# Kernel optimization log

Hardware: AMD Instinct MI355X
Metric: run time of the kernel (lower is better)

## Reference

```python
import jax, jax.numpy as jnp
import numpy as np

B, M, D = 2048, 40, 64          # batch, num fields, embedding dim
HIDDEN = [128, 128, 128]        # CIN layer sizes


def setup_inputs() -> dict:
    key = jax.random.key(0)
    kx, k0, k1, k2 = jax.random.split(key, 4)
    x = jax.random.normal(kx, (B, M, D), dtype=jnp.float32)
    # torch.rand -> uniform [0, 1)
    W0 = jax.random.uniform(k0, (M, M, HIDDEN[0]), dtype=jnp.float32)
    W1 = jax.random.uniform(k1, (M, HIDDEN[0], HIDDEN[1]), dtype=jnp.float32)
    W2 = jax.random.uniform(k2, (M, HIDDEN[1], HIDDEN[2]), dtype=jnp.float32)
    return {"x": x, "W0": W0, "W1": W1, "W2": W2}


def _cin_forward(x, Ws):
    # x: [b, m, d]. Each layer k:
    #   x_next[b, l, d] = sum_{m, h} x0[b, m, d] * x_k[b, h, d] * W_k[m, h, l]
    # which equals the torch 'bil,bjl->bjil' outer product followed by
    # 'bijk,ijl->bkl' + transpose, but expressed as one fused contraction
    # (opt_einsum picks a path avoiding the worst intermediate).
    ps = []
    xk = x  # [b, H_k, d], H_0 = m
    for W in Ws:
        x_next = jnp.einsum('bmd,bhd,mhl->bld', x, xk, W)  # [b, L_k, d]
        ps.append(jnp.sum(x_next, axis=2))                  # [b, L_k]
        xk = x_next
    return jnp.concatenate(ps, axis=1)                      # [b, sum(L_k)]


def reference(x, W0, W1, W2):
    return _cin_forward(x, (W0, W1, W2))
```

## Files before the change

kernel.cpp:

```cpp
#include <hip/hip_runtime.h>
#include <hip/hip_bf16.h>
#include <cstdint>

#define BATCH 2048
#define MF    40
#define DDIM  64
#define LDIM  128
#define ROWS  (BATCH * DDIM)

typedef __attribute__((ext_vector_type(4)))  short    short4_t;
typedef __attribute__((ext_vector_type(8)))  short    short8;
typedef __attribute__((ext_vector_type(8)))  __bf16   bf16x8;
typedef __attribute__((ext_vector_type(2)))  float    floatx2;
typedef __attribute__((ext_vector_type(16))) float    floatx16;

__device__ __forceinline__ unsigned short f32_to_bf16(float f) {
    union { float f; uint32_t u; } v; v.f = f;
    uint32_t u = v.u;
    uint32_t r = (u + 0x7fffu + ((u >> 16) & 1u)) >> 16;
    return (unsigned short)r;
}

__device__ __forceinline__ void barrier_raw() {
    asm volatile("s_barrier" ::: "memory");
}
template <int N> __device__ __forceinline__ void vmwait() {
    if constexpr (N == 0)  asm volatile("s_waitcnt vmcnt(0)"  ::: "memory");
    if constexpr (N == 3)  asm volatile("s_waitcnt vmcnt(3)"  ::: "memory");
    if constexpr (N == 4)  asm volatile("s_waitcnt vmcnt(4)"  ::: "memory");
    if constexpr (N == 10) asm volatile("s_waitcnt vmcnt(10)" ::: "memory");
}

__global__ void k_wprep(const float* __restrict__ W, unsigned short* __restrict__ Wt,
                        int KK, int H) {
    int bi = blockIdx.x;
    int lane = threadIdx.x;
    int cb = bi & 3;
    int mkk = bi >> 2;
    int kk = mkk % KK, m = mkk / KK;
    int l = cb * 32 + (lane & 31);
    int hbase = kk * 16 + (lane >> 5) * 8;
    unsigned short o[8];
#pragma unroll
    for (int j = 0; j < 8; ++j) {
        int h = hbase + j;
        float v = (h < H) ? W[((size_t)m * H + h) * LDIM + l] : 0.f;
        o[j] = f32_to_bf16(v);
    }
    *(short8*)(Wt + ((size_t)bi * 64 + lane) * 8) = *(const short8*)o;
}

template <int KK, int KU, bool FIRST, int OFF, bool WRITEX>
__global__ __launch_bounds__(256, 2) void k_gemm(
    const float* __restrict__ x,
    const unsigned short* __restrict__ Xprev,
    const unsigned short* __restrict__ Wt,
    unsigned short* __restrict__ Xout,
    float* __restrict__ out)
{
    constexpr int UPM   = KK / KU;
    constexpr int NU    = MF * UPM;
    constexpr int SLOTS = (KU == 4) ? 2 : 3;
    constexpr int DIST  = SLOTS;

    __shared__ unsigned short slab[4][KU * 2048];

    const int tid  = threadIdx.x;
    const int lane = tid & 63, wave = tid >> 6;
    const int hf   = lane >> 5, r31 = lane & 31;
    const int rowhalf = wave >> 1, colhalf = wave & 1;
    const int b = blockIdx.x * 2 + rowhalf;

    bf16x8 xk[2][KK];
    if constexpr (FIRST) {
#pragma unroll
        for (int t = 0; t < 2; ++t)
#pragma unroll
            for (int kk = 0; kk < KK; ++kk) {
                unsigned short tmp[8];
#pragma unroll
                for (int j = 0; j < 8; ++j) {
                    int h = kk * 16 + hf * 8 + j;
                    float v = (h < MF) ? x[((size_t)b * MF + h) * DDIM + t * 32 + r31] : 0.f;
                    tmp[j] = f32_to_bf16(v);
                }
                xk[t][kk] = __builtin_bit_cast(bf16x8, *(const short8*)tmp);
            }
    } else {
#pragma unroll
        for (int t = 0; t < 2; ++t)
#pragma unroll
            for (int kk = 0; kk < KK; ++kk)
                xk[t][kk] = __builtin_bit_cast(bf16x8, *(const short8*)(
                    Xprev + (size_t)(b * 64 + t * 32 + r31) * LDIM + kk * 16 + hf * 8));
    }

    floatx16 acc[2][2] = {};

    auto stage = [&](int uu) {
        int u = uu < NU ? uu : NU - 1;
        const unsigned short* src = Wt + (size_t)u * (KU * 2048);
#pragma unroll
        for (int it = 0; it < KU; ++it) {
            int c = it * 256 + tid;
            __builtin_amdgcn_global_load_lds(
                (const __attribute__((address_space(1))) uint32_t*)(src + (size_t)c * 8),
                (__attribute__((address_space(3))) uint32_t*)(&slab[u & 3][(size_t)c * 8]),
                16, 0, 0);
        }
    };

    const int cbg0 = colhalf * 2, cbg1 = colhalf * 2 + 1;
    auto ldfrag = [&](int u, int frag, int cb) {
        return __builtin_bit_cast(bf16x8,
            *(const short8*)(&slab[u & 3][((size_t)(frag * 4 + cb) * 64 + lane) * 8]));
    };

    vmwait<0>();
    stage(0); stage(1); stage(2);
    vmwait<(KU == 4) ? 4 : 3>();
    barrier_raw();

    bf16x8 bbuf[SLOTS][2];
#pragma unroll
    for (int p = 0; p < SLOTS; ++p) {
        bbuf[p][0] = ldfrag(0, p, cbg0);
        bbuf[p][1] = ldfrag(0, p, cbg1);
    }

    float s0v = 0.f, s1v = 0.f;

#pragma unroll 1
    for (int m = 0; m < MF; ++m) {
        floatx16 P[2][2] = {};
#pragma unroll
        for (int kk = 0; kk < KK; ++kk) {
            if (kk % KU == 0) {
                barrier_raw();
                asm volatile("s_setprio 1");
                if (kk == 0) {
                    const float* sp = x + ((size_t)b * MF + m) * DDIM + r31;
                    s0v = sp[0];
                    s1v = sp[32];
                }
                stage(m * UPM + kk / KU + 3);
            }
            const int slot = (KU == 4) ? (kk & 1) : kk;
            P[0][0] = __builtin_amdgcn_mfma_f32_32x32x16_bf16(bbuf[slot][0], xk[0][kk], P[0][0], 0, 0, 0);
            P[1][0] = __builtin_amdgcn_mfma_f32_32x32x16_bf16(bbuf[slot][0], xk[1][kk], P[1][0], 0, 0, 0);
            P[0][1] = __builtin_amdgcn_mfma_f32_32x32x16_bf16(bbuf[slot][1], xk[0][kk], P[0][1], 0, 0, 0);
            P[1][1] = __builtin_amdgcn_mfma_f32_32x32x16_bf16(bbuf[slot][1], xk[1][kk], P[1][1], 0, 0, 0);
            {
                const int j  = kk + DIST;
                int mm = m + ((j >= KK) ? 1 : 0);
                if (mm > MF - 1) mm = MF - 1;
                const int jj = (j >= KK) ? (j - KK) : j;
                const int u  = mm * UPM + jj / KU;
                bbuf[slot][0] = ldfrag(u, jj % KU, cbg0);
                bbuf[slot][1] = ldfrag(u, jj % KU, cbg1);
            }
            if (kk % KU == KU - 1) vmwait<10>();
        }
        asm volatile("s_setprio 0");
#pragma unroll
        for (int t = 0; t < 2; ++t) {
            const float sv = (t == 0) ? s0v : s1v;
            floatx2 s2 = {sv, sv};
#pragma unroll
            for (int cbp = 0; cbp < 2; ++cbp) {
                floatx2*       A = (floatx2*)&acc[t][cbp];
                const floatx2* Q = (const floatx2*)&P[t][cbp];
#pragma unroll
                for (int i = 0; i < 8; ++i) A[i] += s2 * Q[i];
            }
        }
    }

    if constexpr (WRITEX) {
#pragma unroll
        for (int t = 0; t < 2; ++t) {
            const size_t rowbase = (size_t)(b * 64 + t * 32 + r31) * LDIM;
#pragma unroll
            for (int cbp = 0; cbp < 2; ++cbp) {
#pragma unroll
                for (int g = 0; g < 4; ++g) {
                    unsigned short o[4];
#pragma unroll
                    for (int i = 0; i < 4; ++i) o[i] = f32_to_bf16(acc[t][cbp][g * 4 + i]);
                    *(short4_t*)(Xout + rowbase + (colhalf * 2 + cbp) * 32 + 8 * g + 4 * hf) =
                        *(const short4_t*)o;
                }
            }
        }
    }

#pragma unroll
    for (int cbp = 0; cbp < 2; ++cbp) {
#pragma unroll
        for (int j = 0; j < 16; ++j) {
            float v = acc[0][cbp][j] + acc[1][cbp][j];
            v += __shfl_xor(v, 16);
            v += __shfl_xor(v, 8);
            v += __shfl_xor(v, 4);
            v += __shfl_xor(v, 2);
            v += __shfl_xor(v, 1);
            if (r31 == 0)
                out[(size_t)b * 384 + OFF + (colhalf * 2 + cbp) * 32 +
                    (j & 3) + 8 * (j >> 2) + 4 * hf] = v;
        }
    }
}

extern "C" void kernel_launch(void* const* d_in, const int* in_sizes, int n_in,
                              void* d_out, int out_size, void* d_ws, size_t ws_size,
                              hipStream_t stream) {
    const float* x  = (const float*)d_in[0];
    const float* W0 = (const float*)d_in[1];
    const float* W1 = (const float*)d_in[2];
    const float* W2 = (const float*)d_in[3];
    float* out = (float*)d_out;

    char* ws = (char*)d_ws;
    size_t off = 0;
    auto alloc = [&](size_t bytes) -> void* {
        void* p = ws + off;
        off += (bytes + 255) & ~(size_t)255;
        return p;
    };
    unsigned short* W0t = (unsigned short*)alloc((size_t)MF * 3 * 2048 * 2);
    unsigned short* W1t = (unsigned short*)alloc((size_t)MF * 8 * 2048 * 2);
    unsigned short* W2t = (unsigned short*)alloc((size_t)MF * 8 * 2048 * 2);
    unsigned short* X1p = (unsigned short*)alloc((size_t)ROWS * LDIM * 2);
    unsigned short* X2p = (unsigned short*)alloc((size_t)ROWS * LDIM * 2);

    k_wprep<<<MF * 3 * 4, 64, 0, stream>>>(W0, W0t, 3, 40);
    k_wprep<<<MF * 8 * 4, 64, 0, stream>>>(W1, W1t, 8, 128);
    k_wprep<<<MF * 8 * 4, 64, 0, stream>>>(W2, W2t, 8, 128);

    k_gemm<3, 3, true,  0,   true ><<<ROWS / 128, 256, 0, stream>>>(x, nullptr, W0t, X1p, out);
    k_gemm<8, 4, false, 128, true ><<<ROWS / 128, 256, 0, stream>>>(x, X1p,     W1t, X2p, out);
    k_gemm<8, 4, false, 256, false><<<ROWS / 128, 256, 0, stream>>>(x, X2p,     W2t, X2p, out);
}
```

Baseline: 463.2 us.

## Fuse three CIN layers into one kernel with LDS exchange of intermediates

```diff
diff --git a/kernel.cpp b/kernel.cpp
--- a/kernel.cpp
+++ b/kernel.cpp
@@ -24,16 +24,26 @@
 __device__ __forceinline__ void barrier_raw() {
     asm volatile("s_barrier" ::: "memory");
 }
+__device__ __forceinline__ void lgkmwait0() {
+    asm volatile("s_waitcnt lgkmcnt(0)" ::: "memory");
+}
 template <int N> __device__ __forceinline__ void vmwait() {
     if constexpr (N == 0)  asm volatile("s_waitcnt vmcnt(0)"  ::: "memory");
-    if constexpr (N == 3)  asm volatile("s_waitcnt vmcnt(3)"  ::: "memory");
     if constexpr (N == 4)  asm volatile("s_waitcnt vmcnt(4)"  ::: "memory");
+    if constexpr (N == 6)  asm volatile("s_waitcnt vmcnt(6)"  ::: "memory");
     if constexpr (N == 10) asm volatile("s_waitcnt vmcnt(10)" ::: "memory");
 }
 
-__global__ void k_wprep(const float* __restrict__ W, unsigned short* __restrict__ Wt,
-                        int KK, int H) {
+__global__ void k_wprep_all(const float* __restrict__ W0, const float* __restrict__ W1,
+                            const float* __restrict__ W2,
+                            unsigned short* __restrict__ W0t,
+                            unsigned short* __restrict__ W1t,
+                            unsigned short* __restrict__ W2t) {
     int bi = blockIdx.x;
+    const float* W; unsigned short* Wt; int KK, H;
+    if (bi < 640)       { W = W0; Wt = W0t; KK = 4; H = 40; }
+    else if (bi < 1920) { bi -= 640;  W = W1; Wt = W1t; KK = 8; H = 128; }
+    else                { bi -= 1920; W = W2; Wt = W2t; KK = 8; H = 128; }
     int lane = threadIdx.x;
     int cb = bi & 3;
     int mkk = bi >> 2;
@@ -47,83 +57,50 @@
         float v = (h < H) ? W[((size_t)m * H + h) * LDIM + l] : 0.f;
         o[j] = f32_to_bf16(v);
     }
-    *(short8*)(Wt + ((size_t)bi * 64 + lane) * 8) = *(const short8*)o;
-}
-
-template <int KK, int KU, bool FIRST, int OFF, bool WRITEX>
-__global__ __launch_bounds__(256, 2) void k_gemm(
-    const float* __restrict__ x,
-    const unsigned short* __restrict__ Xprev,
+    *(short8*)(Wt + (((size_t)(m * KK + kk) * 4 + cb) * 64 + lane) * 8) = *(const short8*)o;
+}
+
+template <int KK>
+__device__ __forceinline__ void layer_loop(
     const unsigned short* __restrict__ Wt,
-    unsigned short* __restrict__ Xout,
-    float* __restrict__ out)
+    const float* __restrict__ x, int b,
+    int lane, int hf, int r31, int cbg0, int cbg1,
+    unsigned short* slabf,
+    bf16x8 (&xk)[2][8], floatx16 (&acc)[2][2])
 {
-    constexpr int UPM   = KK / KU;
-    constexpr int NU    = MF * UPM;
-    constexpr int SLOTS = (KU == 4) ? 2 : 3;
-    constexpr int DIST  = SLOTS;
-
-    __shared__ unsigned short slab[4][KU * 2048];
-
-    const int tid  = threadIdx.x;
-    const int lane = tid & 63, wave = tid >> 6;
-    const int hf   = lane >> 5, r31 = lane & 31;
-    const int rowhalf = wave >> 1, colhalf = wave & 1;
-    const int b = blockIdx.x * 2 + rowhalf;
-
-    bf16x8 xk[2][KK];
-    if constexpr (FIRST) {
-#pragma unroll
-        for (int t = 0; t < 2; ++t)
-#pragma unroll
-            for (int kk = 0; kk < KK; ++kk) {
-                unsigned short tmp[8];
-#pragma unroll
-                for (int j = 0; j < 8; ++j) {
-                    int h = kk * 16 + hf * 8 + j;
-                    float v = (h < MF) ? x[((size_t)b * MF + h) * DDIM + t * 32 + r31] : 0.f;
-                    tmp[j] = f32_to_bf16(v);
-                }
-                xk[t][kk] = __builtin_bit_cast(bf16x8, *(const short8*)tmp);
-            }
-    } else {
-#pragma unroll
-        for (int t = 0; t < 2; ++t)
-#pragma unroll
-            for (int kk = 0; kk < KK; ++kk)
-                xk[t][kk] = __builtin_bit_cast(bf16x8, *(const short8*)(
-                    Xprev + (size_t)(b * 64 + t * 32 + r31) * LDIM + kk * 16 + hf * 8));
-    }
-
-    floatx16 acc[2][2] = {};
+    constexpr int UPM  = KK / 4;
+    constexpr int NU   = MF * UPM;
+    constexpr int GATE = (KK == 8) ? 10 : 6;
 
     auto stage = [&](int uu) {
         int u = uu < NU ? uu : NU - 1;
-        const unsigned short* src = Wt + (size_t)u * (KU * 2048);
-#pragma unroll
-        for (int it = 0; it < KU; ++it) {
+        const unsigned short* src = Wt + (size_t)u * 8192;
+        const int tid = threadIdx.x;
+#pragma unroll
+        for (int it = 0; it < 4; ++it) {
             int c = it * 256 + tid;
             __builtin_amdgcn_global_load_lds(
                 (const __attribute__((address_space(1))) uint32_t*)(src + (size_t)c * 8),
-                (__attribute__((address_space(3))) uint32_t*)(&slab[u & 3][(size_t)c * 8]),
+                (__attribute__((address_space(3))) uint32_t*)(&slabf[(size_t)(u & 3) * 8192 + (size_t)c * 8]),
                 16, 0, 0);
         }
     };
-
-    const int cbg0 = colhalf * 2, cbg1 = colhalf * 2 + 1;
     auto ldfrag = [&](int u, int frag, int cb) {
-        return __builtin_bit_cast(bf16x8,
-            *(const short8*)(&slab[u & 3][((size_t)(frag * 4 + cb) * 64 + lane) * 8]));
-    };
+        return __builtin_bit_cast(bf16x8, *(const short8*)(
+            &slabf[(size_t)(u & 3) * 8192 + ((size_t)(frag * 4 + cb) * 64 + lane) * 8]));
+    };
+
+    acc[0][0] = floatx16{}; acc[0][1] = floatx16{};
+    acc[1][0] = floatx16{}; acc[1][1] = floatx16{};
 
     vmwait<0>();
     stage(0); stage(1); stage(2);
-    vmwait<(KU == 4) ? 4 : 3>();
+    vmwait<4>();
     barrier_raw();
 
-    bf16x8 bbuf[SLOTS][2];
-#pragma unroll
-    for (int p = 0; p < SLOTS; ++p) {
+    bf16x8 bbuf[2][2];
+#pragma unroll
+    for (int p = 0; p < 2; ++p) {
         bbuf[p][0] = ldfrag(0, p, cbg0);
         bbuf[p][1] = ldfrag(0, p, cbg1);
     }
@@ -135,7 +112,7 @@
         floatx16 P[2][2] = {};
 #pragma unroll
         for (int kk = 0; kk < KK; ++kk) {
-            if (kk % KU == 0) {
+            if (kk % 4 == 0) {
                 barrier_raw();
                 asm volatile("s_setprio 1");
                 if (kk == 0) {
@@ -143,23 +120,23 @@
                     s0v = sp[0];
                     s1v = sp[32];
                 }
-                stage(m * UPM + kk / KU + 3);
-            }
-            const int slot = (KU == 4) ? (kk & 1) : kk;
+                stage(m * UPM + kk / 4 + 3);
+            }
+            const int slot = kk & 1;
             P[0][0] = __builtin_amdgcn_mfma_f32_32x32x16_bf16(bbuf[slot][0], xk[0][kk], P[0][0], 0, 0, 0);
             P[1][0] = __builtin_amdgcn_mfma_f32_32x32x16_bf16(bbuf[slot][0], xk[1][kk], P[1][0], 0, 0, 0);
             P[0][1] = __builtin_amdgcn_mfma_f32_32x32x16_bf16(bbuf[slot][1], xk[0][kk], P[0][1], 0, 0, 0);
             P[1][1] = __builtin_amdgcn_mfma_f32_32x32x16_bf16(bbuf[slot][1], xk[1][kk], P[1][1], 0, 0, 0);
             {
-                const int j  = kk + DIST;
+                const int j  = kk + 2;
                 int mm = m + ((j >= KK) ? 1 : 0);
                 if (mm > MF - 1) mm = MF - 1;
                 const int jj = (j >= KK) ? (j - KK) : j;
-                const int u  = mm * UPM + jj / KU;
-                bbuf[slot][0] = ldfrag(u, jj % KU, cbg0);
-                bbuf[slot][1] = ldfrag(u, jj % KU, cbg1);
-            }
-            if (kk % KU == KU - 1) vmwait<10>();
+                const int u  = mm * UPM + jj / 4;
+                bbuf[slot][0] = ldfrag(u, jj % 4, cbg0);
+                bbuf[slot][1] = ldfrag(u, jj % 4, cbg1);
+            }
+            if (kk % 4 == 3) vmwait<GATE>();
         }
         asm volatile("s_setprio 0");
 #pragma unroll
@@ -175,40 +152,100 @@
             }
         }
     }
-
-    if constexpr (WRITEX) {
-#pragma unroll
-        for (int t = 0; t < 2; ++t) {
-            const size_t rowbase = (size_t)(b * 64 + t * 32 + r31) * LDIM;
-#pragma unroll
-            for (int cbp = 0; cbp < 2; ++cbp) {
+}
+
+__global__ __launch_bounds__(256, 2) void k_cin(
+    const float* __restrict__ x,
+    const unsigned short* __restrict__ W0t,
+    const unsigned short* __restrict__ W1t,
+    const unsigned short* __restrict__ W2t,
+    float* __restrict__ out)
+{
+    __shared__ unsigned short slab[4][8192];
+    unsigned short* slabf = &slab[0][0];
+
+    const int tid  = threadIdx.x;
+    const int lane = tid & 63, wave = tid >> 6;
+    const int hf   = lane >> 5, r31 = lane & 31;
+    const int rowhalf = wave >> 1, colhalf = wave & 1;
+    const int b = blockIdx.x * 2 + rowhalf;
+    const int cbg0 = colhalf * 2, cbg1 = colhalf * 2 + 1;
+
+    bf16x8   xk[2][8];
+    floatx16 acc[2][2];
+
+    auto write_ps = [&](int OFF) {
+#pragma unroll
+        for (int cbp = 0; cbp < 2; ++cbp) {
+#pragma unroll
+            for (int j = 0; j < 16; ++j) {
+                float v = acc[0][cbp][j] + acc[1][cbp][j];
+                v += __shfl_xor(v, 16);
+                v += __shfl_xor(v, 8);
+                v += __shfl_xor(v, 4);
+                v += __shfl_xor(v, 2);
+                v += __shfl_xor(v, 1);
+                if (r31 == 0)
+                    out[(size_t)b * 384 + OFF + (colhalf * 2 + cbp) * 32 +
+                        (j & 3) + 8 * (j >> 2) + 4 * hf] = v;
+            }
+        }
+    };
+
+    auto exchange = [&]() {
+        vmwait<0>();
+        barrier_raw();
+#pragma unroll
+        for (int t = 0; t < 2; ++t)
+#pragma unroll
+            for (int cbp = 0; cbp < 2; ++cbp)
 #pragma unroll
                 for (int g = 0; g < 4; ++g) {
                     unsigned short o[4];
 #pragma unroll
                     for (int i = 0; i < 4; ++i) o[i] = f32_to_bf16(acc[t][cbp][g * 4 + i]);
-                    *(short4_t*)(Xout + rowbase + (colhalf * 2 + cbp) * 32 + 8 * g + 4 * hf) =
+                    const int kk  = colhalf * 4 + cbp * 2 + (g >> 1);
+                    const int hfr = g & 1;
+                    *(short4_t*)(&slabf[(size_t)rowhalf * 8192 +
+                        ((size_t)(t * 8 + kk) * 64 + hfr * 32 + r31) * 8 + 4 * hf]) =
                         *(const short4_t*)o;
                 }
-            }
-        }
-    }
-
-#pragma unroll
-    for (int cbp = 0; cbp < 2; ++cbp) {
-#pragma unroll
-        for (int j = 0; j < 16; ++j) {
-            float v = acc[0][cbp][j] + acc[1][cbp][j];
-            v += __shfl_xor(v, 16);
-            v += __shfl_xor(v, 8);
-            v += __shfl_xor(v, 4);
-            v += __shfl_xor(v, 2);
-            v += __shfl_xor(v, 1);
-            if (r31 == 0)
-                out[(size_t)b * 384 + OFF + (colhalf * 2 + cbp) * 32 +
-                    (j & 3) + 8 * (j >> 2) + 4 * hf] = v;
-        }
-    }
+        lgkmwait0();
+        barrier_raw();
+#pragma unroll
+        for (int t = 0; t < 2; ++t)
+#pragma unroll
+            for (int kk = 0; kk < 8; ++kk)
+                xk[t][kk] = __builtin_bit_cast(bf16x8, *(const short8*)(
+                    &slabf[(size_t)rowhalf * 8192 + ((size_t)(t * 8 + kk) * 64 + lane) * 8]));
+        lgkmwait0();
+        barrier_raw();
+    };
+
+#pragma unroll
+    for (int t = 0; t < 2; ++t)
+#pragma unroll
+        for (int kk = 0; kk < 4; ++kk) {
+            unsigned short tmp[8];
+#pragma unroll
+            for (int j = 0; j < 8; ++j) {
+                int h = kk * 16 + hf * 8 + j;
+                float v = (h < MF) ? x[((size_t)b * MF + h) * DDIM + t * 32 + r31] : 0.f;
+                tmp[j] = f32_to_bf16(v);
+            }
+            xk[t][kk] = __builtin_bit_cast(bf16x8, *(const short8*)tmp);
+        }
+
+    layer_loop<4>(W0t, x, b, lane, hf, r31, cbg0, cbg1, slabf, xk, acc);
+    write_ps(0);
+    exchange();
+
+    layer_loop<8>(W1t, x, b, lane, hf, r31, cbg0, cbg1, slabf, xk, acc);
+    write_ps(128);
+    exchange();
+
+    layer_loop<8>(W2t, x, b, lane, hf, r31, cbg0, cbg1, slabf, xk, acc);
+    write_ps(256);
 }
 
 extern "C" void kernel_launch(void* const* d_in, const int* in_sizes, int n_in,
@@ -227,17 +264,10 @@
         off += (bytes + 255) & ~(size_t)255;
         return p;
     };
-    unsigned short* W0t = (unsigned short*)alloc((size_t)MF * 3 * 2048 * 2);
+    unsigned short* W0t = (unsigned short*)alloc((size_t)MF * 4 * 2048 * 2);
     unsigned short* W1t = (unsigned short*)alloc((size_t)MF * 8 * 2048 * 2);
     unsigned short* W2t = (unsigned short*)alloc((size_t)MF * 8 * 2048 * 2);
-    unsigned short* X1p = (unsigned short*)alloc((size_t)ROWS * LDIM * 2);
-    unsigned short* X2p = (unsigned short*)alloc((size_t)ROWS * LDIM * 2);
-
-    k_wprep<<<MF * 3 * 4, 64, 0, stream>>>(W0, W0t, 3, 40);
-    k_wprep<<<MF * 8 * 4, 64, 0, stream>>>(W1, W1t, 8, 128);
-    k_wprep<<<MF * 8 * 4, 64, 0, stream>>>(W2, W2t, 8, 128);
-
-    k_gemm<3, 3, true,  0,   true ><<<ROWS / 128, 256, 0, stream>>>(x, nullptr, W0t, X1p, out);
-    k_gemm<8, 4, false, 128, true ><<<ROWS / 128, 256, 0, stream>>>(x, X1p,     W1t, X2p, out);
-    k_gemm<8, 4, false, 256, false><<<ROWS / 128, 256, 0, stream>>>(x, X2p,     W2t, X2p, out);
-}
+
+    k_wprep_all<<<3200, 64, 0, stream>>>(W0, W1, W2, W0t, W1t, W2t);
+    k_cin<<<ROWS / 128, 256, 0, stream>>>(x, W0t, W1t, W2t, out);
+}
```

After: 438.7 us. 5.3% less time.
